# Optimization experiments

Hardware: AMD Instinct MI355X
Metric: run time of the kernel (lower is better)

The kernel has to match this reference:

```python
import jax, jax.numpy as jnp
import numpy as np

B, N, E, D, H, L = 1024, 64, 1024, 128, 4, 2
C = D // H          # per-head out_channels
K = 5               # options per attribute
LN_EPS = 1e-5


def setup_inputs() -> dict:
    key = jax.random.key(0)
    ks = jax.random.split(key, 22)
    s = 0.05
    inp = {
        'x': jax.random.randint(ks[0], (B, N), 0, K),
        'edge_index': jax.random.randint(ks[1], (2, E), 0, N),
        'edge_attr': jax.random.uniform(ks[2], (E, 1), jnp.float32),
        # tokenizer params
        'attr_emb': jax.random.normal(ks[3], (N, D), jnp.float32) * s,
        'opt_emb': jax.random.normal(ks[4], (N, K, D), jnp.float32) * s,
        'prior': jnp.ones((N, 1), jnp.float32),
        # GATv2 params, stacked over layers
        'Wl': jax.random.normal(ks[5], (L, D, D), jnp.float32) * s,
        'bl': jnp.zeros((L, D), jnp.float32),
        'Wr': jax.random.normal(ks[6], (L, D, D), jnp.float32) * s,
        'br': jnp.zeros((L, D), jnp.float32),
        'We': jax.random.normal(ks[7], (L, 1, D), jnp.float32) * s,
        'att': jax.random.normal(ks[8], (L, H, C), jnp.float32) * s,
        'conv_bias': jnp.zeros((L, D), jnp.float32),
        'ln_g': jnp.ones((L, D), jnp.float32),
        'ln_b': jnp.zeros((L, D), jnp.float32),
        # reliability head
        'W1': jax.random.normal(ks[9], (2 * D, D), jnp.float32) * s,
        'b1': jnp.zeros((D,), jnp.float32),
        'W2': jax.random.normal(ks[10], (D, 1), jnp.float32) * s,
        'b2': jnp.zeros((1,), jnp.float32),
    }
    return inp


def _forward(x, edge_index, edge_attr, attr_emb, opt_emb, prior,
             Wl, bl, Wr, br, We, att, conv_bias, ln_g, ln_b, W1, b1, W2, b2):
    Bb, n = x.shape
    # Tokenizer: token_i = p_i * (E_attr[i] + E_val[i](x_i))
    val = opt_emb[jnp.arange(n)[None, :], x]                 # [B,n,D]
    T0 = (attr_emb[None] + val) * prior[None]                # [B,n,D]

    src, dst = edge_index[0], edge_index[1]
    h = T0
    for l in range(Wl.shape[0]):
        xl = (h @ Wl[l] + bl[l]).reshape(Bb, n, H, C)        # source transform
        xr = (h @ Wr[l] + br[l]).reshape(Bb, n, H, C)        # target transform
        e = (edge_attr @ We[l]).reshape(1, E, H, C)          # edge embedding
        msg = xl[:, src]                                     # [B,E,H,C]
        z = jax.nn.leaky_relu(msg + xr[:, dst] + e, 0.2)
        alpha = jnp.einsum('behc,hc->beh', z, att[l])        # [B,E,H]
        # segment softmax over incoming edges per target node
        mx = jnp.full((Bb, n, H), -jnp.inf, alpha.dtype).at[:, dst].max(alpha)
        ex = jnp.exp(alpha - mx[:, dst])
        den = jnp.zeros((Bb, n, H), alpha.dtype).at[:, dst].add(ex)
        a = ex / den[:, dst]                                 # normalized attention
        out = jnp.zeros((Bb, n, H, C), h.dtype).at[:, dst].add(msg * a[..., None])
        g = out.reshape(Bb, n, D) + conv_bias[l]
        mu = g.mean(-1, keepdims=True)
        var = g.var(-1, keepdims=True)
        g = (g - mu) / jnp.sqrt(var + LN_EPS) * ln_g[l] + ln_b[l]
        g = jax.nn.elu(g)
        h = h + g                                            # residual

    hat_T = jnp.concatenate([T0, h], axis=-1)                # [B,n,2D]
    rel = jax.nn.sigmoid(jax.nn.relu(hat_T @ W1 + b1) @ W2 + b2)[..., 0]  # [B,n]
    rw = rel[..., None]
    f_scale = (h * rw).sum(1) / (rw.sum(1) + 1e-8)           # [B,D]
    return f_scale, rel, hat_T


def reference(x, edge_index, edge_attr, attr_emb, opt_emb, prior,
              Wl, bl, Wr, br, We, att, conv_bias, ln_g, ln_b, W1, b1, W2, b2):
    return _forward(x, edge_index, edge_attr, attr_emb, opt_emb, prior,
                    Wl, bl, Wr, br, We, att, conv_bias, ln_g, ln_b, W1, b1, W2, b2)
```

## Files before the change

kernel.cpp:

```cpp
#include <hip/hip_runtime.h>
#include <hip/hip_bf16.h>

#define Bv 1024
#define Nv 64
#define Ev 1024
#define Dv 128
#define Hv 4
#define Lv 2
#define Kv 5
#define PAD 136

typedef __hip_bfloat16 bf16;
typedef __attribute__((ext_vector_type(8))) short bf16x8_t;
typedef __attribute__((ext_vector_type(4))) float f32x4_t;
typedef __attribute__((ext_vector_type(2))) float f32x2_t;

__device__ __forceinline__ float b2f(bf16 v) { return __bfloat162float(v); }
__device__ __forceinline__ bf16  f2b(float v) { return __float2bfloat16(v); }

__device__ bf16 g_pWl[(size_t)Lv * 2 * Dv * Dv];
__device__ bf16 g_pWr[(size_t)Lv * 2 * Dv * Dv];
__device__ bf16 g_pW1[(size_t)2 * 2 * Dv * Dv];
__device__ float g_K[Lv * Hv];
__device__ unsigned int g_etab[Ev];
__device__ int          g_off[Nv + 1];

__device__ __forceinline__ f32x2_t unpack2v(unsigned int u) {
    union { unsigned int u; float f; } a, b;
    a.u = u << 16;
    b.u = u & 0xffff0000u;
    return (f32x2_t){a.f, b.f};
}

__device__ __forceinline__ unsigned int pack2v(f32x2_t v) {
    union { bf16 b; unsigned short u; } lo, hi;
    lo.b = f2b(v.x); hi.b = f2b(v.y);
    return (unsigned int)lo.u | ((unsigned int)hi.u << 16);
}

__device__ __forceinline__ bf16x8_t load8(const bf16* p, int elem) {
    return *(const bf16x8_t*)(p + elem);
}
union b8u { bf16x8_t v; unsigned int u[4]; };

__device__ void pack_mat(const float* __restrict__ W, bf16* __restrict__ out,
                         int K, int tid, int nth)
{
    const int total = K * 128;
    for (int e = tid; e < total; e += nth) {
        int f    = e >> 9;
        int rem  = e & 511;
        int lane = rem >> 3;
        int i    = rem & 7;
        int kk   = f >> 3;
        int nt   = f & 7;
        int col  = nt * 16 + (lane & 15);
        int k    = kk * 32 + (lane >> 4) * 8 + i;
        float w  = W[k * 128 + col];
        bf16 hi  = f2b(w);
        out[e]         = hi;
        out[total + e] = f2b(w - b2f(hi));
    }
}

__global__ void prep(const int* __restrict__ edge_index, const float* __restrict__ edge_attr,
                     const float* __restrict__ Wl, const float* __restrict__ Wr,
                     const float* __restrict__ W1, const float* __restrict__ We,
                     const float* __restrict__ att)
{
    const int bid = blockIdx.x;
    if (bid == 0) {
        __shared__ int cnt[Nv];
        int tid = threadIdx.x;
        if (tid < Nv) cnt[tid] = 0;
        __syncthreads();
        for (int e = tid; e < Ev; e += blockDim.x)
            atomicAdd(&cnt[edge_index[Ev + e]], 1);
        __syncthreads();
        if (tid == 0) {
            int s = 0;
            for (int t = 0; t < Nv; ++t) { int c = cnt[t]; g_off[t] = s; cnt[t] = s; s += c; }
            g_off[Nv] = s;
        }
        __syncthreads();
        for (int e = tid; e < Ev; e += blockDim.x) {
            int s = edge_index[e];
            int d = edge_index[Ev + e];
            int pos = atomicAdd(&cnt[d], 1);
            union { bf16 b; unsigned short u; } cv;
            cv.b = f2b(edge_attr[e]);
            g_etab[pos] = (unsigned int)(s | (d << 6)) | ((unsigned int)cv.u << 16);
        }
        return;
    }
    const int nth = (gridDim.x - 1) * 256;
    const int tid = (bid - 1) * 256 + threadIdx.x;
    for (int l = 0; l < Lv; ++l) {
        pack_mat(Wl + (size_t)l * Dv * Dv, g_pWl + (size_t)l * 2 * Dv * Dv, Dv, tid, nth);
        pack_mat(Wr + (size_t)l * Dv * Dv, g_pWr + (size_t)l * 2 * Dv * Dv, Dv, tid, nth);
    }
    pack_mat(W1, g_pW1, 2 * Dv, tid, nth);
    if (bid == 1 && threadIdx.x < Lv * Hv) {
        int l = threadIdx.x / Hv, h = threadIdx.x % Hv;
        float k = 0.f;
        for (int c = 0; c < 32; ++c)
            k += att[l * Dv + h * 32 + c] * We[l * Dv + h * 32 + c];
        g_K[threadIdx.x] = 0.2f * k;
    }
}

__global__ __launch_bounds__(512, 2)
void gat_fused(const int* __restrict__ x,
               const float* __restrict__ attr_emb,
               const float* __restrict__ opt_emb, const float* __restrict__ prior,
               const float* __restrict__ bl, const float* __restrict__ br,
               const float* __restrict__ conv_bias, const float* __restrict__ ln_g,
               const float* __restrict__ ln_b,
               const float* __restrict__ b1, const float* __restrict__ W2,
               const float* __restrict__ b2,
               const float* __restrict__ We, const float* __restrict__ att,
               float* __restrict__ out_fscale, float* __restrict__ out_rel,
               float* __restrict__ out_hatT)
{
    const int b = blockIdx.x;
    const int tid = threadIdx.x;

    __shared__ __align__(16) bf16 hs [Nv * PAD];
    __shared__ __align__(16) bf16 xls[Nv * PAD];
    __shared__ __align__(16) bf16 xrs[Nv * PAD];
    __shared__ __align__(16) bf16 alphas[Ev * Hv];
    __shared__ __align__(16) float red [Nv * 8];
    __shared__ __align__(16) float red2[Nv * 8];
    __shared__ __align__(16) float watt[256];
    __shared__ __align__(16) float w2col[Dv];
    __shared__ float relbuf[Nv];

    const int my_t  = tid & 63;
    const int beg   = g_off[my_t];
    const int end   = g_off[my_t + 1];

    for (int idx = tid; idx < Nv * Dv; idx += 512) {
        int n = idx >> 7, d = idx & 127;
        float t0 = (attr_emb[n * Dv + d] + opt_emb[(n * Kv + x[b * Nv + n]) * Dv + d])
                   * prior[n];
        hs[n * PAD + d] = f2b(t0);
    }

    for (int l = 0; l < Lv; ++l) {
        if (tid < 256) {
            int h = tid >> 6, cp = (tid >> 2) & 15, e = tid & 3;
            int c = cp * 2 + (e & 1);
            watt[tid] = (e < 2) ? We[l * Dv + h * 32 + c] : att[l * Dv + h * 32 + c];
        }
        __syncthreads();

        {
            const int w = tid >> 6, lane = tid & 63;
            const int row16 = lane & 15, kg = lane >> 4;
            const bf16* pB = (w < 4) ? (g_pWl + (size_t)l * 2 * Dv * Dv)
                                     : (g_pWr + (size_t)l * 2 * Dv * Dv);
            const int wc = (w & 3) * 32;
            bf16* dst = (w < 4) ? xls : xrs;
            const float* bias = (w < 4) ? (bl + l * Dv) : (br + l * Dv);

            #pragma unroll
            for (int nt = 0; nt < 2; ++nt) {
                f32x4_t acc[4];
                #pragma unroll
                for (int mt = 0; mt < 4; ++mt)
                    acc[mt] = (f32x4_t){0.f, 0.f, 0.f, 0.f};

                #pragma unroll
                for (int kk = 0; kk < 4; ++kk) {
                    const int kb = kk * 32 + kg * 8;
                    const int f = kk * 8 + (w & 3) * 2 + nt;
                    bf16x8_t bh  = *(const bf16x8_t*)&pB[(size_t)(f * 64 + lane) * 8];
                    bf16x8_t blo = *(const bf16x8_t*)&pB[Dv * Dv + (size_t)(f * 64 + lane) * 8];
                    #pragma unroll
                    for (int mt = 0; mt < 4; ++mt) {
                        bf16x8_t a = load8(hs, (mt * 16 + row16) * PAD + kb);
                        acc[mt] = __builtin_amdgcn_mfma_f32_16x16x32_bf16(a, bh,  acc[mt], 0, 0, 0);
                        acc[mt] = __builtin_amdgcn_mfma_f32_16x16x32_bf16(a, blo, acc[mt], 0, 0, 0);
                    }
                }
                const int col = wc + nt * 16 + row16;
                const float bv = bias[col];
                #pragma unroll
                for (int mt = 0; mt < 4; ++mt) {
                    #pragma unroll
                    for (int r = 0; r < 4; ++r) {
                        const int row = mt * 16 + kg * 4 + r;
                        dst[row * PAD + col] = f2b(acc[mt][r] + bv);
                    }
                }
            }
        }
        __syncthreads();

        {
            const int t = tid & 63, h = (tid >> 6) & 3, half = tid >> 8;
            const int ch0 = h * 32 + half * 16;
            b8u a0, a1;
            a0.v = load8(xls, t * PAD + ch0);
            a1.v = load8(xls, t * PAD + ch0 + 8);
            f32x2_t dl2 = {0.f, 0.f};
            #pragma unroll
            for (int j = 0; j < 4; ++j) {
                f32x2_t at2 = *(const f32x2_t*)&watt[h * 64 + (half * 8 + j) * 4 + 2];
                dl2 += at2 * unpack2v(a0.u[j]);
            }
            #pragma unroll
            for (int j = 0; j < 4; ++j) {
                f32x2_t at2 = *(const f32x2_t*)&watt[h * 64 + (half * 8 + 4 + j) * 4 + 2];
                dl2 += at2 * unpack2v(a1.u[j]);
            }
            red[t * 8 + h * 2 + half] = dl2.x + dl2.y;
        }
        __syncthreads();

        {
            const int h = (tid >> 6) & 3, half = tid >> 8, lane = tid & 63;
            const float k02 = g_K[l * Hv + h];
            const f32x2_t zero2 = {0.f, 0.f};
            unsigned int ets[8];
            #pragma unroll
            for (int e = 0; e < 8; ++e)
                ets[e] = g_etab[(half * 8 + e) * 64 + lane];
            f32x2_t acc[8];
            #pragma unroll
            for (int e = 0; e < 8; ++e) acc[e] = (f32x2_t){0.f, 0.f};

            #pragma unroll
            for (int q = 0; q < 4; ++q) {
                f32x4_t wa[4];
                #pragma unroll
                for (int j = 0; j < 4; ++j)
                    wa[j] = *(const f32x4_t*)&watt[h * 64 + (q * 4 + j) * 4];
                #pragma unroll
                for (int e = 0; e < 8; ++e) {
                    int s = ets[e] & 63, t = (ets[e] >> 6) & 63;
                    b8u xl, xr;
                    xl.v = load8(xls, s * PAD + h * 32 + q * 8);
                    xr.v = load8(xrs, t * PAD + h * 32 + q * 8);
                    union { unsigned int u; float f; } ec; ec.u = ets[e] & 0xffff0000u;
                    f32x2_t ea2 = {ec.f, ec.f};
                    #pragma unroll
                    for (int j = 0; j < 4; ++j) {
                        f32x2_t xl2 = unpack2v(xl.u[j]);
                        f32x2_t xr2 = unpack2v(xr.u[j]);
                        f32x2_t we2 = {wa[j].x, wa[j].y};
                        f32x2_t at2 = {wa[j].z, wa[j].w};
                        f32x2_t v   = xl2 + xr2 + ea2 * we2;
                        acc[e] += at2 * __builtin_elementwise_max(v, zero2);
                    }
                }
            }
            #pragma unroll
            for (int e = 0; e < 8; ++e) {
                int s = ets[e] & 63;
                union { unsigned int u; float f; } ec; ec.u = ets[e] & 0xffff0000u;
                float dL = red[s * 8 + h * 2] + red[s * 8 + h * 2 + 1];
                float alpha = 0.2f * dL + k02 * ec.f + 0.8f * (acc[e].x + acc[e].y);
                alphas[((half * 8 + e) * 64 + lane) * Hv + h] = f2b(alpha);
            }
        }
        __syncthreads();

        {
            const int t = my_t, h = (tid >> 6) & 3, half = tid >> 8;
            const int ch0 = h * 32 + half * 16;
            float mx = -3e38f;
            for (int idx = beg; idx < end; ++idx)
                mx = fmaxf(mx, b2f(alphas[idx * Hv + h]));
            f32x2_t acc2[8];
            #pragma unroll
            for (int j = 0; j < 8; ++j) acc2[j] = (f32x2_t){0.f, 0.f};
            float den = 0.f;
            for (int idx = beg; idx < end; ++idx) {
                int s = (int)(g_etab[idx] & 63u);
                float ex = expf(b2f(alphas[idx * Hv + h]) - mx);
                den += ex;
                f32x2_t ex2 = {ex, ex};
                b8u m0, m1;
                m0.v = load8(xls, s * PAD + ch0);
                m1.v = load8(xls, s * PAD + ch0 + 8);
                #pragma unroll
                for (int j = 0; j < 4; ++j)
                    acc2[j] += ex2 * unpack2v(m0.u[j]);
                #pragma unroll
                for (int j = 0; j < 4; ++j)
                    acc2[4 + j] += ex2 * unpack2v(m1.u[j]);
            }
            float inv_den = (end > beg) ? 1.f / den : 0.f;
            f32x2_t id2 = {inv_den, inv_den};
            f32x2_t sum2 = {0.f, 0.f}, sq2 = {0.f, 0.f};
            #pragma unroll
            for (int j = 0; j < 8; ++j) {
                f32x2_t cb = *(const f32x2_t*)&conv_bias[l * Dv + ch0 + 2 * j];
                f32x2_t g  = acc2[j] * id2 + cb;
                acc2[j] = g;
                sum2 += g; sq2 += g * g;
            }
            red [t * 8 + h * 2 + half] = sum2.x + sum2.y;
            red2[t * 8 + h * 2 + half] = sq2.x + sq2.y;
            __syncthreads();
            float mu = 0.f, ms = 0.f;
            #pragma unroll
            for (int j = 0; j < 8; ++j) { mu += red[t * 8 + j]; ms += red2[t * 8 + j]; }
            mu *= (1.f / 128.f); ms *= (1.f / 128.f);
            float rstd = rsqrtf(ms - mu * mu + 1e-5f);
            f32x2_t mu2 = {mu, mu}, rs2 = {rstd, rstd};
            #pragma unroll
            for (int j = 0; j < 8; ++j) {
                f32x2_t lg = *(const f32x2_t*)&ln_g[l * Dv + ch0 + 2 * j];
                f32x2_t lb = *(const f32x2_t*)&ln_b[l * Dv + ch0 + 2 * j];
                f32x2_t g  = (acc2[j] - mu2) * rs2 * lg + lb;
                g.x = g.x > 0.f ? g.x : (expf(g.x) - 1.f);
                g.y = g.y > 0.f ? g.y : (expf(g.y) - 1.f);
                unsigned int* hp = (unsigned int*)&hs[t * PAD + ch0 + 2 * j];
                f32x2_t hv = unpack2v(*hp) + g;
                *hp = pack2v(hv);
            }
        }
        __syncthreads();
    }

    if (tid < Dv) w2col[tid] = W2[tid];
    for (int idx = tid; idx < Nv * Dv; idx += 512) {
        int n = idx >> 7, d = idx & 127;
        float t0 = (attr_emb[n * Dv + d] + opt_emb[(n * Kv + x[b * Nv + n]) * Dv + d])
                   * prior[n];
        xrs[n * PAD + d] = f2b(t0);
        size_t rb = ((size_t)(b * Nv + n)) * (2 * Dv);
        out_hatT[rb + d]      = t0;
        out_hatT[rb + Dv + d] = b2f(hs[n * PAD + d]);
    }
    __syncthreads();

    {
        const int w = tid >> 6, lane = tid & 63;
        const int row16 = lane & 15, kg = lane >> 4;
        f32x4_t acc[4];
        #pragma unroll
        for (int mt = 0; mt < 4; ++mt)
            acc[mt] = (f32x4_t){0.f, 0.f, 0.f, 0.f};

        #pragma unroll
        for (int kk = 0; kk < 8; ++kk) {
            const bf16* asrc = (kk < 4) ? xrs : hs;
            const int kb = (kk & 3) * 32 + kg * 8;
            const int f = kk * 8 + w;
            bf16x8_t bh  = *(const bf16x8_t*)&g_pW1[(size_t)(f * 64 + lane) * 8];
            bf16x8_t blo = *(const bf16x8_t*)&g_pW1[(size_t)2 * Dv * Dv + (size_t)(f * 64 + lane) * 8];
            #pragma unroll
            for (int mt = 0; mt < 4; ++mt) {
                bf16x8_t a = load8(asrc, (mt * 16 + row16) * PAD + kb);
                acc[mt] = __builtin_amdgcn_mfma_f32_16x16x32_bf16(a, bh,  acc[mt], 0, 0, 0);
                acc[mt] = __builtin_amdgcn_mfma_f32_16x16x32_bf16(a, blo, acc[mt], 0, 0, 0);
            }
        }
        #pragma unroll
        for (int mt = 0; mt < 4; ++mt) {
            const int col = w * 16 + row16;
            #pragma unroll
            for (int r = 0; r < 4; ++r) {
                const int row = mt * 16 + kg * 4 + r;
                float v = acc[mt][r] + b1[col];
                xls[row * PAD + col] = f2b(v > 0.f ? v : 0.f);
            }
        }
    }
    __syncthreads();

    {
        const int t = tid & 63, h = (tid >> 6) & 3, half = tid >> 8;
        const int ch0 = h * 32 + half * 16;
        b8u h0, h1;
        h0.v = load8(xls, t * PAD + ch0);
        h1.v = load8(xls, t * PAD + ch0 + 8);
        f32x2_t s2 = {0.f, 0.f};
        #pragma unroll
        for (int j = 0; j < 4; ++j)
            s2 += unpack2v(h0.u[j]) * *(const f32x2_t*)&w2col[ch0 + 2 * j];
        #pragma unroll
        for (int j = 0; j < 4; ++j)
            s2 += unpack2v(h1.u[j]) * *(const f32x2_t*)&w2col[ch0 + 8 + 2 * j];
        red[t * 8 + h * 2 + half] = s2.x + s2.y;
        __syncthreads();
        if (h == 0 && half == 0) {
            float z = b2[0];
            #pragma unroll
            for (int j = 0; j < 8; ++j) z += red[t * 8 + j];
            float r = 1.f / (1.f + expf(-z));
            relbuf[t] = r;
            out_rel[b * Nv + t] = r;
        }
    }
    __syncthreads();

    if (tid < Dv) {
        float num = 0.f, den = 0.f;
        for (int n = 0; n < Nv; ++n) {
            float r = relbuf[n];
            num += b2f(hs[n * PAD + tid]) * r;
            den += r;
        }
        out_fscale[b * Dv + tid] = num / (den + 1e-8f);
    }
}

extern "C" void kernel_launch(void* const* d_in, const int* in_sizes, int n_in,
                              void* d_out, int out_size, void* d_ws, size_t ws_size,
                              hipStream_t stream)
{
    const int*   x          = (const int*)  d_in[0];
    const int*   edge_index = (const int*)  d_in[1];
    const float* edge_attr  = (const float*)d_in[2];
    const float* attr_emb   = (const float*)d_in[3];
    const float* opt_emb    = (const float*)d_in[4];
    const float* prior      = (const float*)d_in[5];
    const float* Wl         = (const float*)d_in[6];
    const float* bl         = (const float*)d_in[7];
    const float* Wr         = (const float*)d_in[8];
    const float* br         = (const float*)d_in[9];
    const float* We         = (const float*)d_in[10];
    const float* att        = (const float*)d_in[11];
    const float* conv_bias  = (const float*)d_in[12];
    const float* ln_g       = (const float*)d_in[13];
    const float* ln_b       = (const float*)d_in[14];
    const float* W1         = (const float*)d_in[15];
    const float* b1         = (const float*)d_in[16];
    const float* W2         = (const float*)d_in[17];
    const float* b2         = (const float*)d_in[18];

    float* out        = (float*)d_out;
    float* out_fscale = out;
    float* out_rel    = out + (size_t)Bv * Dv;
    float* out_hatT   = out + (size_t)Bv * Dv + (size_t)Bv * Nv;

    prep<<<129, 256, 0, stream>>>(edge_index, edge_attr, Wl, Wr, W1, We, att);
    gat_fused<<<Bv, 512, 0, stream>>>(x, attr_emb, opt_emb,
                                      prior, bl, br, conv_bias,
                                      ln_g, ln_b, b1, W2, b2, We, att,
                                      out_fscale, out_rel, out_hatT);
}
```

Baseline: 279.5 us.

## Process two batch elements per block to reuse weights and edge metadata

Each 512-thread block now handles two batch samples instead of one, and the grid is halved. Weight fragments for the MFMA GEMMs, the edge table entries, the attention parameters and the per-node offsets are loaded once and applied to both samples, which also gives more independent work per thread to hide latency. In exchange LDS use roughly doubles (about 90KB per block) and register pressure rises, which can lower occupancy under launch_bounds(512,2). The grid shrinks to 512 blocks, fewer than two per CU on a 256-CU part, so tail balance and latency hiding may get worse.

```diff
diff --git a/kernel.cpp b/kernel.cpp
--- a/kernel.cpp
+++ b/kernel.cpp
@@ -122,28 +122,32 @@
                float* __restrict__ out_fscale, float* __restrict__ out_rel,
                float* __restrict__ out_hatT)
 {
-    const int b = blockIdx.x;
+    const int b0  = blockIdx.x * 2;
     const int tid = threadIdx.x;
 
-    __shared__ __align__(16) bf16 hs [Nv * PAD];
-    __shared__ __align__(16) bf16 xls[Nv * PAD];
-    __shared__ __align__(16) bf16 xrs[Nv * PAD];
-    __shared__ __align__(16) bf16 alphas[Ev * Hv];
-    __shared__ __align__(16) float red [Nv * 8];
-    __shared__ __align__(16) float red2[Nv * 8];
+    __shared__ __align__(16) bf16 hs [2][Nv * PAD];
+    __shared__ __align__(16) bf16 xls[2][Nv * PAD];
+    __shared__ __align__(16) bf16 xrs[2][Nv * PAD];
+    __shared__ __align__(16) bf16 alphas[2][Ev * Hv];
+    __shared__ __align__(16) float red [2][Nv * 8];
+    __shared__ __align__(16) float red2[2][Nv * 8];
     __shared__ __align__(16) float watt[256];
     __shared__ __align__(16) float w2col[Dv];
-    __shared__ float relbuf[Nv];
-
-    const int my_t  = tid & 63;
-    const int beg   = g_off[my_t];
-    const int end   = g_off[my_t + 1];
+    __shared__ float relbuf[2][Nv];
+
+    const int my_t = tid & 63;
+    const int beg  = g_off[my_t];
+    const int end  = g_off[my_t + 1];
 
     for (int idx = tid; idx < Nv * Dv; idx += 512) {
         int n = idx >> 7, d = idx & 127;
-        float t0 = (attr_emb[n * Dv + d] + opt_emb[(n * Kv + x[b * Nv + n]) * Dv + d])
-                   * prior[n];
-        hs[n * PAD + d] = f2b(t0);
+        float ae = attr_emb[n * Dv + d];
+        float pr = prior[n];
+        #pragma unroll
+        for (int el = 0; el < 2; ++el) {
+            float t0 = (ae + opt_emb[(n * Kv + x[(b0 + el) * Nv + n]) * Dv + d]) * pr;
+            hs[el][n * PAD + d] = f2b(t0);
+        }
     }
 
     for (int l = 0; l < Lv; ++l) {
@@ -160,15 +164,16 @@
             const bf16* pB = (w < 4) ? (g_pWl + (size_t)l * 2 * Dv * Dv)
                                      : (g_pWr + (size_t)l * 2 * Dv * Dv);
             const int wc = (w & 3) * 32;
-            bf16* dst = (w < 4) ? xls : xrs;
             const float* bias = (w < 4) ? (bl + l * Dv) : (br + l * Dv);
 
             #pragma unroll
             for (int nt = 0; nt < 2; ++nt) {
-                f32x4_t acc[4];
-                #pragma unroll
-                for (int mt = 0; mt < 4; ++mt)
-                    acc[mt] = (f32x4_t){0.f, 0.f, 0.f, 0.f};
+                f32x4_t acc[2][4];
+                #pragma unroll
+                for (int el = 0; el < 2; ++el)
+                    #pragma unroll
+                    for (int mt = 0; mt < 4; ++mt)
+                        acc[el][mt] = (f32x4_t){0.f, 0.f, 0.f, 0.f};
 
                 #pragma unroll
                 for (int kk = 0; kk < 4; ++kk) {
@@ -178,19 +183,26 @@
                     bf16x8_t blo = *(const bf16x8_t*)&pB[Dv * Dv + (size_t)(f * 64 + lane) * 8];
                     #pragma unroll
                     for (int mt = 0; mt < 4; ++mt) {
-                        bf16x8_t a = load8(hs, (mt * 16 + row16) * PAD + kb);
-                        acc[mt] = __builtin_amdgcn_mfma_f32_16x16x32_bf16(a, bh,  acc[mt], 0, 0, 0);
-                        acc[mt] = __builtin_amdgcn_mfma_f32_16x16x32_bf16(a, blo, acc[mt], 0, 0, 0);
+                        #pragma unroll
+                        for (int el = 0; el < 2; ++el) {
+                            bf16x8_t a = load8(hs[el], (mt * 16 + row16) * PAD + kb);
+                            acc[el][mt] = __builtin_amdgcn_mfma_f32_16x16x32_bf16(a, bh,  acc[el][mt], 0, 0, 0);
+                            acc[el][mt] = __builtin_amdgcn_mfma_f32_16x16x32_bf16(a, blo, acc[el][mt], 0, 0, 0);
+                        }
                     }
                 }
                 const int col = wc + nt * 16 + row16;
                 const float bv = bias[col];
                 #pragma unroll
-                for (int mt = 0; mt < 4; ++mt) {
+                for (int el = 0; el < 2; ++el) {
+                    bf16* dst = (w < 4) ? xls[el] : xrs[el];
                     #pragma unroll
-                    for (int r = 0; r < 4; ++r) {
-                        const int row = mt * 16 + kg * 4 + r;
-                        dst[row * PAD + col] = f2b(acc[mt][r] + bv);
+                    for (int mt = 0; mt < 4; ++mt) {
+                        #pragma unroll
+                        for (int r = 0; r < 4; ++r) {
+                            const int row = mt * 16 + kg * 4 + r;
+                            dst[row * PAD + col] = f2b(acc[el][mt][r] + bv);
+                        }
                     }
                 }
             }
@@ -200,21 +212,24 @@
         {
             const int t = tid & 63, h = (tid >> 6) & 3, half = tid >> 8;
             const int ch0 = h * 32 + half * 16;
-            b8u a0, a1;
-            a0.v = load8(xls, t * PAD + ch0);
-            a1.v = load8(xls, t * PAD + ch0 + 8);
-            f32x2_t dl2 = {0.f, 0.f};
-            #pragma unroll
-            for (int j = 0; j < 4; ++j) {
-                f32x2_t at2 = *(const f32x2_t*)&watt[h * 64 + (half * 8 + j) * 4 + 2];
-                dl2 += at2 * unpack2v(a0.u[j]);
-            }
-            #pragma unroll
-            for (int j = 0; j < 4; ++j) {
-                f32x2_t at2 = *(const f32x2_t*)&watt[h * 64 + (half * 8 + 4 + j) * 4 + 2];
-                dl2 += at2 * unpack2v(a1.u[j]);
-            }
-            red[t * 8 + h * 2 + half] = dl2.x + dl2.y;
+            #pragma unroll
+            for (int el = 0; el < 2; ++el) {
+                b8u a0, a1;
+                a0.v = load8(xls[el], t * PAD + ch0);
+                a1.v = load8(xls[el], t * PAD + ch0 + 8);
+                f32x2_t dl2 = {0.f, 0.f};
+                #pragma unroll
+                for (int j = 0; j < 4; ++j) {
+                    f32x2_t at2 = *(const f32x2_t*)&watt[h * 64 + (half * 8 + j) * 4 + 2];
+                    dl2 += at2 * unpack2v(a0.u[j]);
+                }
+                #pragma unroll
+                for (int j = 0; j < 4; ++j) {
+                    f32x2_t at2 = *(const f32x2_t*)&watt[h * 64 + (half * 8 + 4 + j) * 4 + 2];
+                    dl2 += at2 * unpack2v(a1.u[j]);
+                }
+                red[el][t * 8 + h * 2 + half] = dl2.x + dl2.y;
+            }
         }
         __syncthreads();
 
@@ -226,9 +241,11 @@
             #pragma unroll
             for (int e = 0; e < 8; ++e)
                 ets[e] = g_etab[(half * 8 + e) * 64 + lane];
-            f32x2_t acc[8];
-            #pragma unroll
-            for (int e = 0; e < 8; ++e) acc[e] = (f32x2_t){0.f, 0.f};
+            f32x2_t acc[2][8];
+            #pragma unroll
+            for (int el = 0; el < 2; ++el)
+                #pragma unroll
+                for (int e = 0; e < 8; ++e) acc[el][e] = (f32x2_t){0.f, 0.f};
 
             #pragma unroll
             for (int q = 0; q < 4; ++q) {
@@ -239,19 +256,22 @@
                 #pragma unroll
                 for (int e = 0; e < 8; ++e) {
                     int s = ets[e] & 63, t = (ets[e] >> 6) & 63;
-                    b8u xl, xr;
-                    xl.v = load8(xls, s * PAD + h * 32 + q * 8);
-                    xr.v = load8(xrs, t * PAD + h * 32 + q * 8);
                     union { unsigned int u; float f; } ec; ec.u = ets[e] & 0xffff0000u;
                     f32x2_t ea2 = {ec.f, ec.f};
                     #pragma unroll
-                    for (int j = 0; j < 4; ++j) {
-                        f32x2_t xl2 = unpack2v(xl.u[j]);
-                        f32x2_t xr2 = unpack2v(xr.u[j]);
-                        f32x2_t we2 = {wa[j].x, wa[j].y};
-                        f32x2_t at2 = {wa[j].z, wa[j].w};
-                        f32x2_t v   = xl2 + xr2 + ea2 * we2;
-                        acc[e] += at2 * __builtin_elementwise_max(v, zero2);
+                    for (int el = 0; el < 2; ++el) {
+                        b8u xl, xr;
+                        xl.v = load8(xls[el], s * PAD + h * 32 + q * 8);
+                        xr.v = load8(xrs[el], t * PAD + h * 32 + q * 8);
+                        #pragma unroll
+                        for (int j = 0; j < 4; ++j) {
+                            f32x2_t xl2 = unpack2v(xl.u[j]);
+                            f32x2_t xr2 = unpack2v(xr.u[j]);
+                            f32x2_t we2 = {wa[j].x, wa[j].y};
+                            f32x2_t at2 = {wa[j].z, wa[j].w};
+                            f32x2_t v   = xl2 + xr2 + ea2 * we2;
+                            acc[el][e] += at2 * __builtin_elementwise_max(v, zero2);
+                        }
                     }
                 }
             }
@@ -259,9 +279,12 @@
             for (int e = 0; e < 8; ++e) {
                 int s = ets[e] & 63;
                 union { unsigned int u; float f; } ec; ec.u = ets[e] & 0xffff0000u;
-                float dL = red[s * 8 + h * 2] + red[s * 8 + h * 2 + 1];
-                float alpha = 0.2f * dL + k02 * ec.f + 0.8f * (acc[e].x + acc[e].y);
-                alphas[((half * 8 + e) * 64 + lane) * Hv + h] = f2b(alpha);
+                #pragma unroll
+                for (int el = 0; el < 2; ++el) {
+                    float dL = red[el][s * 8 + h * 2] + red[el][s * 8 + h * 2 + 1];
+                    float alpha = 0.2f * dL + k02 * ec.f + 0.8f * (acc[el][e].x + acc[el][e].y);
+                    alphas[el][((half * 8 + e) * 64 + lane) * Hv + h] = f2b(alpha);
+                }
             }
         }
         __syncthreads();
@@ -269,57 +292,84 @@
         {
             const int t = my_t, h = (tid >> 6) & 3, half = tid >> 8;
             const int ch0 = h * 32 + half * 16;
-            float mx = -3e38f;
-            for (int idx = beg; idx < end; ++idx)
-                mx = fmaxf(mx, b2f(alphas[idx * Hv + h]));
-            f32x2_t acc2[8];
-            #pragma unroll
-            for (int j = 0; j < 8; ++j) acc2[j] = (f32x2_t){0.f, 0.f};
-            float den = 0.f;
+            float mx[2] = {-3e38f, -3e38f};
+            for (int idx = beg; idx < end; ++idx) {
+                #pragma unroll
+                for (int el = 0; el < 2; ++el)
+                    mx[el] = fmaxf(mx[el], b2f(alphas[el][idx * Hv + h]));
+            }
+            f32x2_t acc2[2][8];
+            #pragma unroll
+            for (int el = 0; el < 2; ++el)
+                #pragma unroll
+                for (int j = 0; j < 8; ++j) acc2[el][j] = (f32x2_t){0.f, 0.f};
+            float den[2] = {0.f, 0.f};
             for (int idx = beg; idx < end; ++idx) {
                 int s = (int)(g_etab[idx] & 63u);
-                float ex = expf(b2f(alphas[idx * Hv + h]) - mx);
-                den += ex;
-                f32x2_t ex2 = {ex, ex};
-                b8u m0, m1;
-                m0.v = load8(xls, s * PAD + ch0);
-                m1.v = load8(xls, s * PAD + ch0 + 8);
-                #pragma unroll
-                for (int j = 0; j < 4; ++j)
-                    acc2[j] += ex2 * unpack2v(m0.u[j]);
-                #pragma unroll
-                for (int j = 0; j < 4; ++j)
-                    acc2[4 + j] += ex2 * unpack2v(m1.u[j]);
-            }
-            float inv_den = (end > beg) ? 1.f / den : 0.f;
-            f32x2_t id2 = {inv_den, inv_den};
-            f32x2_t sum2 = {0.f, 0.f}, sq2 = {0.f, 0.f};
+                #pragma unroll
+                for (int el = 0; el < 2; ++el) {
+                    float ex = expf(b2f(alphas[el][idx * Hv + h]) - mx[el]);
+                    den[el] += ex;
+                    f32x2_t ex2 = {ex, ex};
+                    b8u m0, m1;
+                    m0.v = load8(xls[el], s * PAD + ch0);
+                    m1.v = load8(xls[el], s * PAD + ch0 + 8);
+                    #pragma unroll
+                    for (int j = 0; j < 4; ++j)
+                        acc2[el][j] += ex2 * unpack2v(m0.u[j]);
+                    #pragma unroll
+                    for (int j = 0; j < 4; ++j)
+                        acc2[el][4 + j] += ex2 * unpack2v(m1.u[j]);
+                }
+            }
+            f32x2_t id2[2], sum2[2], sq2[2];
+            #pragma unroll
+            for (int el = 0; el < 2; ++el) {
+                float inv_den = (end > beg) ? 1.f / den[el] : 0.f;
+                id2[el] = (f32x2_t){inv_den, inv_den};
+                sum2[el] = (f32x2_t){0.f, 0.f};
+                sq2[el]  = (f32x2_t){0.f, 0.f};
+            }
             #pragma unroll
             for (int j = 0; j < 8; ++j) {
                 f32x2_t cb = *(const f32x2_t*)&conv_bias[l * Dv + ch0 + 2 * j];
-                f32x2_t g  = acc2[j] * id2 + cb;
-                acc2[j] = g;
-                sum2 += g; sq2 += g * g;
-            }
-            red [t * 8 + h * 2 + half] = sum2.x + sum2.y;
-            red2[t * 8 + h * 2 + half] = sq2.x + sq2.y;
+                #pragma unroll
+                for (int el = 0; el < 2; ++el) {
+                    f32x2_t g = acc2[el][j] * id2[el] + cb;
+                    acc2[el][j] = g;
+                    sum2[el] += g; sq2[el] += g * g;
+                }
+            }
+            #pragma unroll
+            for (int el = 0; el < 2; ++el) {
+                red [el][t * 8 + h * 2 + half] = sum2[el].x + sum2[el].y;
+                red2[el][t * 8 + h * 2 + half] = sq2[el].x + sq2[el].y;
+            }
             __syncthreads();
-            float mu = 0.f, ms = 0.f;
-            #pragma unroll
-            for (int j = 0; j < 8; ++j) { mu += red[t * 8 + j]; ms += red2[t * 8 + j]; }
-            mu *= (1.f / 128.f); ms *= (1.f / 128.f);
-            float rstd = rsqrtf(ms - mu * mu + 1e-5f);
-            f32x2_t mu2 = {mu, mu}, rs2 = {rstd, rstd};
+            f32x2_t mu2[2], rs2[2];
+            #pragma unroll
+            for (int el = 0; el < 2; ++el) {
+                float mu = 0.f, ms = 0.f;
+                #pragma unroll
+                for (int j = 0; j < 8; ++j) { mu += red[el][t * 8 + j]; ms += red2[el][t * 8 + j]; }
+                mu *= (1.f / 128.f); ms *= (1.f / 128.f);
+                float rstd = rsqrtf(ms - mu * mu + 1e-5f);
+                mu2[el] = (f32x2_t){mu, mu};
+                rs2[el] = (f32x2_t){rstd, rstd};
+            }
             #pragma unroll
             for (int j = 0; j < 8; ++j) {
                 f32x2_t lg = *(const f32x2_t*)&ln_g[l * Dv + ch0 + 2 * j];
                 f32x2_t lb = *(const f32x2_t*)&ln_b[l * Dv + ch0 + 2 * j];
-                f32x2_t g  = (acc2[j] - mu2) * rs2 * lg + lb;
-                g.x = g.x > 0.f ? g.x : (expf(g.x) - 1.f);
-                g.y = g.y > 0.f ? g.y : (expf(g.y) - 1.f);
-                unsigned int* hp = (unsigned int*)&hs[t * PAD + ch0 + 2 * j];
-                f32x2_t hv = unpack2v(*hp) + g;
-                *hp = pack2v(hv);
+                #pragma unroll
+                for (int el = 0; el < 2; ++el) {
+                    f32x2_t g = (acc2[el][j] - mu2[el]) * rs2[el] * lg + lb;
+                    g.x = g.x > 0.f ? g.x : (expf(g.x) - 1.f);
+                    g.y = g.y > 0.f ? g.y : (expf(g.y) - 1.f);
+                    unsigned int* hp = (unsigned int*)&hs[el][t * PAD + ch0 + 2 * j];
+                    f32x2_t hv = unpack2v(*hp) + g;
+                    *hp = pack2v(hv);
+                }
             }
         }
         __syncthreads();
@@ -328,45 +378,59 @@
     if (tid < Dv) w2col[tid] = W2[tid];
     for (int idx = tid; idx < Nv * Dv; idx += 512) {
         int n = idx >> 7, d = idx & 127;
-        float t0 = (attr_emb[n * Dv + d] + opt_emb[(n * Kv + x[b * Nv + n]) * Dv + d])
-                   * prior[n];
-        xrs[n * PAD + d] = f2b(t0);
-        size_t rb = ((size_t)(b * Nv + n)) * (2 * Dv);
-        out_hatT[rb + d]      = t0;
-        out_hatT[rb + Dv + d] = b2f(hs[n * PAD + d]);
+        float ae = attr_emb[n * Dv + d];
+        float pr = prior[n];
+        #pragma unroll
+        for (int el = 0; el < 2; ++el) {
+            int bb = b0 + el;
+            float t0 = (ae + opt_emb[(n * Kv + x[bb * Nv + n]) * Dv + d]) * pr;
+            xrs[el][n * PAD + d] = f2b(t0);
+            size_t rb = ((size_t)(bb * Nv + n)) * (2 * Dv);
+            out_hatT[rb + d]      = t0;
+            out_hatT[rb + Dv + d] = b2f(hs[el][n * PAD + d]);
+        }
     }
     __syncthreads();
 
     {
         const int w = tid >> 6, lane = tid & 63;
         const int row16 = lane & 15, kg = lane >> 4;
-        f32x4_t acc[4];
-        #pragma unroll
-        for (int mt = 0; mt < 4; ++mt)
-            acc[mt] = (f32x4_t){0.f, 0.f, 0.f, 0.f};
+        f32x4_t acc[2][4];
+        #pragma unroll
+        for (int el = 0; el < 2; ++el)
+            #pragma unroll
+            for (int mt = 0; mt < 4; ++mt)
+                acc[el][mt] = (f32x4_t){0.f, 0.f, 0.f, 0.f};
 
         #pragma unroll
         for (int kk = 0; kk < 8; ++kk) {
-            const bf16* asrc = (kk < 4) ? xrs : hs;
             const int kb = (kk & 3) * 32 + kg * 8;
             const int f = kk * 8 + w;
             bf16x8_t bh  = *(const bf16x8_t*)&g_pW1[(size_t)(f * 64 + lane) * 8];
             bf16x8_t blo = *(const bf16x8_t*)&g_pW1[(size_t)2 * Dv * Dv + (size_t)(f * 64 + lane) * 8];
             #pragma unroll
             for (int mt = 0; mt < 4; ++mt) {
-                bf16x8_t a = load8(asrc, (mt * 16 + row16) * PAD + kb);
-                acc[mt] = __builtin_amdgcn_mfma_f32_16x16x32_bf16(a, bh,  acc[mt], 0, 0, 0);
-                acc[mt] = __builtin_amdgcn_mfma_f32_16x16x32_bf16(a, blo, acc[mt], 0, 0, 0);
-            }
-        }
-        #pragma unroll
-        for (int mt = 0; mt < 4; ++mt) {
-            const int col = w * 16 + row16;
-            #pragma unroll
-            for (int r = 0; r < 4; ++r) {
-                const int row = mt * 16 + kg * 4 + r;
-                float v = acc[mt][r] + b1[col];
-                xls[row * PAD + col] = f2b(v > 0.f ? v : 0.f);
+                #pragma unroll
+                for (int el = 0; el < 2; ++el) {
+                    const bf16* asrc = (kk < 4) ? xrs[el] : hs[el];
+                    bf16x8_t a = load8(asrc, (mt * 16 + row16) * PAD + kb);
+                    acc[el][mt] = __builtin_amdgcn_mfma_f32_16x16x32_bf16(a, bh,  acc[el][mt], 0, 0, 0);
+                    acc[el][mt] = __builtin_amdgcn_mfma_f32_16x16x32_bf16(a, blo, acc[el][mt], 0, 0, 0);
+                }
+            }
+        }
+        const int col = w * 16 + row16;
+        const float bv = b1[col];
+        #pragma unroll
+        for (int el = 0; el < 2; ++el) {
+            #pragma unroll
+            for (int mt = 0; mt < 4; ++mt) {
+                #pragma unroll
+                for (int r = 0; r < 4; ++r) {
+                    const int row = mt * 16 + kg * 4 + r;
+                    float v = acc[el][mt][r] + bv;
+                    xls[el][row * PAD + col] = f2b(v > 0.f ? v : 0.f);
+                }
             }
         }
     }
@@ -375,37 +439,46 @@
     {
         const int t = tid & 63, h = (tid >> 6) & 3, half = tid >> 8;
         const int ch0 = h * 32 + half * 16;
-        b8u h0, h1;
-        h0.v = load8(xls, t * PAD + ch0);
-        h1.v = load8(xls, t * PAD + ch0 + 8);
-        f32x2_t s2 = {0.f, 0.f};
-        #pragma unroll
-        for (int j = 0; j < 4; ++j)
-            s2 += unpack2v(h0.u[j]) * *(const f32x2_t*)&w2col[ch0 + 2 * j];
-        #pragma unroll
-        for (int j = 0; j < 4; ++j)
-            s2 += unpack2v(h1.u[j]) * *(const f32x2_t*)&w2col[ch0 + 8 + 2 * j];
-        red[t * 8 + h * 2 + half] = s2.x + s2.y;
+        #pragma unroll
+        for (int el = 0; el < 2; ++el) {
+            b8u h0, h1;
+            h0.v = load8(xls[el], t * PAD + ch0);
+            h1.v = load8(xls[el], t * PAD + ch0 + 8);
+            f32x2_t s2 = {0.f, 0.f};
+            #pragma unroll
+            for (int j = 0; j < 4; ++j)
+                s2 += unpack2v(h0.u[j]) * *(const f32x2_t*)&w2col[ch0 + 2 * j];
+            #pragma unroll
+            for (int j = 0; j < 4; ++j)
+                s2 += unpack2v(h1.u[j]) * *(const f32x2_t*)&w2col[ch0 + 8 + 2 * j];
+            red[el][t * 8 + h * 2 + half] = s2.x + s2.y;
+        }
         __syncthreads();
         if (h == 0 && half == 0) {
-            float z = b2[0];
-            #pragma unroll
-            for (int j = 0; j < 8; ++j) z += red[t * 8 + j];
-            float r = 1.f / (1.f + expf(-z));
-            relbuf[t] = r;
-            out_rel[b * Nv + t] = r;
+            #pragma unroll
+            for (int el = 0; el < 2; ++el) {
+                float z = b2[0];
+                #pragma unroll
+                for (int j = 0; j < 8; ++j) z += red[el][t * 8 + j];
+                float r = 1.f / (1.f + expf(-z));
+                relbuf[el][t] = r;
+                out_rel[(b0 + el) * Nv + t] = r;
+            }
         }
     }
     __syncthreads();
 
     if (tid < Dv) {
-        float num = 0.f, den = 0.f;
-        for (int n = 0; n < Nv; ++n) {
-            float r = relbuf[n];
-            num += b2f(hs[n * PAD + tid]) * r;
-            den += r;
-        }
-        out_fscale[b * Dv + tid] = num / (den + 1e-8f);
+        #pragma unroll
+        for (int el = 0; el < 2; ++el) {
+            float num = 0.f, den = 0.f;
+            for (int n = 0; n < Nv; ++n) {
+                float r = relbuf[el][n];
+                num += b2f(hs[el][n * PAD + tid]) * r;
+                den += r;
+            }
+            out_fscale[(b0 + el) * Dv + tid] = num / (den + 1e-8f);
+        }
     }
 }
 
@@ -439,8 +512,8 @@
     float* out_hatT   = out + (size_t)Bv * Dv + (size_t)Bv * Nv;
 
     prep<<<129, 256, 0, stream>>>(edge_index, edge_attr, Wl, Wr, W1, We, att);
-    gat_fused<<<Bv, 512, 0, stream>>>(x, attr_emb, opt_emb,
-                                      prior, bl, br, conv_bias,
-                                      ln_g, ln_b, b1, W2, b2, We, att,
-                                      out_fscale, out_rel, out_hatT);
-}
+    gat_fused<<<Bv / 2, 512, 0, stream>>>(x, attr_emb, opt_emb,
+                                          prior, bl, br, conv_bias,
+                                          ln_g, ln_b, b1, W2, b2, We, att,
+                                          out_fscale, out_rel, out_hatT);
+}
```

Result: slower. 290.4 us (+3.9%).
